# Kernel tuning notes

Measured on AMD Instinct MI355X. Metric: run time of the kernel, lower is better.

## Reference

```python
import jax, jax.numpy as jnp
import numpy as np

NU, NI, D, LAYERS, NNZ = 50000, 50000, 256, 2, 400000
N = NU + NI
LEAKY_ALPHA = 0.2  # tf.nn.leaky_relu default


def setup_inputs() -> dict:
    key = jax.random.key(0)
    ks = jax.random.split(key, 32)
    inp = {}
    inp["initial_ebs"] = jax.random.normal(ks[0], (N, D), jnp.float32) * 0.1
    for i, nm in enumerate(["W_side_u", "W_dot_u", "W_side_i", "W_dot_i"]):
        inp[nm] = jax.random.normal(ks[1 + i], (LAYERS, D, D), jnp.float32) / np.float32(np.sqrt(D))
    vi = 5
    for ent, ne in (("u", NU), ("i", NI)):
        for mat in ("LI", "L"):
            inp[f"{mat}_vals_{ent}"] = jax.random.uniform(ks[vi], (NNZ,), jnp.float32); vi += 1
            inp[f"{mat}_rows_{ent}"] = jnp.sort(jax.random.randint(ks[vi], (NNZ,), 0, ne, jnp.int32)); vi += 1
            inp[f"{mat}_cols_{ent}"] = jax.random.randint(ks[vi], (NNZ,), 0, N, jnp.int32); vi += 1
    return inp


def _spmm(rows, cols, vals, ebs, n_rows):
    # sparse [n_rows, N] @ dense [N, D] via gather + segment-sum
    return jax.ops.segment_sum(vals[:, None] * ebs[cols], rows, num_segments=n_rows)


def reference(initial_ebs, W_side_u, W_dot_u, W_side_i, W_dot_i,
              LI_vals_u, L_vals_u, LI_vals_i, L_vals_i,
              LI_rows_u, LI_cols_u, L_rows_u, L_cols_u,
              LI_rows_i, LI_cols_i, L_rows_i, L_cols_i):
    ebs = initial_ebs
    layers_ebs = []
    for l in range(LAYERS):
        # entity 'u': rows [0, NU)
        li_u = _spmm(LI_rows_u, LI_cols_u, LI_vals_u, ebs, NU)
        l_u = _spmm(L_rows_u, L_cols_u, L_vals_u, ebs, NU)
        fold_u = jax.nn.leaky_relu(li_u @ W_side_u[l] + (l_u * ebs[:NU]) @ W_dot_u[l], LEAKY_ALPHA)
        # entity 'i': rows [NU, N)
        li_i = _spmm(LI_rows_i, LI_cols_i, LI_vals_i, ebs, NI)
        l_i = _spmm(L_rows_i, L_cols_i, L_vals_i, ebs, NI)
        fold_i = jax.nn.leaky_relu(li_i @ W_side_i[l] + (l_i * ebs[NU:]) @ W_dot_i[l], LEAKY_ALPHA)
        ebs = jnp.concatenate([fold_u, fold_i], axis=0)  # [N, D]
        layers_ebs.append(ebs)
    return jnp.concatenate(layers_ebs, axis=0)  # [LAYERS*N, D]
```

## Files before the change

kernel.cpp:

```cpp
#include <hip/hip_runtime.h>

#define NUQ 50000
#define NIQ 50000
#define DQ 256
#define NTOT 100000
#define LALPHA 0.2f
#define GPE 782

typedef __attribute__((ext_vector_type(8))) __bf16 bf16x8;
typedef __attribute__((ext_vector_type(4))) float floatx4;
typedef __attribute__((ext_vector_type(8))) unsigned short ushort8;

__device__ __forceinline__ float b2f(unsigned short u) {
    unsigned int x = ((unsigned int)u) << 16;
    return __builtin_bit_cast(float, x);
}
__device__ __forceinline__ unsigned short f2b(float f) {
    unsigned int u = __builtin_bit_cast(unsigned int, f);
    u = u + 0x7FFFu + ((u >> 16) & 1u);
    return (unsigned short)(u >> 16);
}

#define GLD_LDS16(g, l)                                                        \
    __builtin_amdgcn_global_load_lds(                                          \
        (const __attribute__((address_space(1))) void*)(g),                    \
        (__attribute__((address_space(3))) void*)(l), 16, 0, 0)

__global__ __launch_bounds__(256) void build_rowptr(
    const int* __restrict__ rows, int nnz, int* __restrict__ rptr, int n_rows)
{
    int e = blockIdx.x * 256 + threadIdx.x;
    if (e > nnz) return;
    int prev = (e == 0)   ? -1     : rows[e - 1];
    int cur  = (e == nnz) ? n_rows : rows[e];
    for (int r = prev + 1; r <= cur; ++r) rptr[r] = e;
}

__global__ __launch_bounds__(256) void cvt_f32_bf16(
    const float* __restrict__ in, unsigned short* __restrict__ out, int n4)
{
    int i = blockIdx.x * 256 + threadIdx.x;
    if (i >= n4) return;
    float4 v = ((const float4*)in)[i];
    ushort4 o;
    o.x = f2b(v.x); o.y = f2b(v.y); o.z = f2b(v.z); o.w = f2b(v.w);
    ((ushort4*)out)[i] = o;
}

__global__ __launch_bounds__(256) void build_bt(
    const float* __restrict__ Ws_u, const float* __restrict__ Wd_u,
    const float* __restrict__ Ws_i, const float* __restrict__ Wd_i,
    unsigned short* __restrict__ Bt)
{
    int idx = blockIdx.x * 256 + threadIdx.x;
    int k   = idx & 511;
    int n   = (idx >> 9) & 255;
    int buf = idx >> 17;
    int l = buf >> 1, e = buf & 1;
    const float* Wside = e ? Ws_i : Ws_u;
    const float* Wdot  = e ? Wd_i : Wd_u;
    float v = (k < 256) ? Wside[((size_t)l * 256 + k)       * 256 + n]
                        : Wdot [((size_t)l * 256 + (k-256)) * 256 + n];
    Bt[idx] = f2b(v);
}

__global__ __launch_bounds__(256) void spmm_merged_v3(
    const int* __restrict__ rpA_u, const int* __restrict__ cA_u, const float* __restrict__ vA_u,
    const int* __restrict__ rpB_u, const int* __restrict__ cB_u, const float* __restrict__ vB_u,
    const int* __restrict__ rpA_i, const int* __restrict__ cA_i, const float* __restrict__ vA_i,
    const int* __restrict__ rpB_i, const int* __restrict__ cB_i, const float* __restrict__ vB_i,
    const unsigned short* __restrict__ src,
    unsigned short* __restrict__ out)
{
    const int wave = threadIdx.x >> 6;
    const int lane = threadIdx.x & 63;
    const int r    = __builtin_amdgcn_readfirstlane(blockIdx.x * 4 + wave);
    const bool isI = (r >= NUQ);
    const int  row = isI ? (r - NUQ) : r;

    const int*   rpA = isI ? rpA_i : rpA_u;
    const int*   cAp = isI ? cA_i  : cA_u;
    const float* vAp = isI ? vA_i  : vA_u;
    const int*   rpB = isI ? rpB_i : rpB_u;
    const int*   cBp = isI ? cB_i  : cB_u;
    const float* vBp = isI ? vB_i  : vB_u;

    const int sA = rpA[row], eA = rpA[row + 1];
    const int sB = rpB[row], eB = rpB[row + 1];

    const int half = lane >> 5;
    const int li   = lane & 31;

    float accA[8] = {0.f, 0.f, 0.f, 0.f, 0.f, 0.f, 0.f, 0.f};
    float accB[8] = {0.f, 0.f, 0.f, 0.f, 0.f, 0.f, 0.f, 0.f};

    int baseA = sA, baseB = sB;
    while (baseA < eA || baseB < eB) {
        int cntA = eA - baseA; cntA = cntA < 0 ? 0 : (cntA > 64 ? 64 : cntA);
        int cntB = eB - baseB; cntB = cntB < 0 ? 0 : (cntB > 64 ? 64 : cntB);
        int mycA = 0; float myvA = 0.f;
        if (lane < cntA) { mycA = cAp[baseA + lane]; myvA = vAp[baseA + lane]; }
        int mycB = 0; float myvB = 0.f;
        if (lane < cntB) { mycB = cBp[baseB + lane]; myvB = vBp[baseB + lane]; }
        const int mx = cntA > cntB ? cntA : cntB;
        #pragma unroll 2
        for (int e = 0; e < mx; e += 2) {
            if (e < cntA) {
                const int   c = __shfl(mycA, e + half, 64);
                const float v = __shfl(myvA, e + half, 64);
                const ushort8 s = *(const ushort8*)(src + (size_t)c * DQ + li * 8);
                #pragma unroll
                for (int j = 0; j < 8; ++j) accA[j] = fmaf(v, b2f(s[j]), accA[j]);
            }
            if (e < cntB) {
                const int   c = __shfl(mycB, e + half, 64);
                const float v = __shfl(myvB, e + half, 64);
                const ushort8 s = *(const ushort8*)(src + (size_t)c * DQ + li * 8);
                #pragma unroll
                for (int j = 0; j < 8; ++j) accB[j] = fmaf(v, b2f(s[j]), accB[j]);
            }
        }
        baseA += 64; baseB += 64;
    }

    #pragma unroll
    for (int j = 0; j < 8; ++j) accA[j] += __shfl_xor(accA[j], 32, 64);
    #pragma unroll
    for (int j = 0; j < 8; ++j) accB[j] += __shfl_xor(accB[j], 32, 64);

    float vo[8];
    if (half == 0) {
        #pragma unroll
        for (int j = 0; j < 8; ++j) vo[j] = accA[j];
    } else {
        const ushort8 m = *(const ushort8*)(src + (size_t)r * DQ + li * 8);
        #pragma unroll
        for (int j = 0; j < 8; ++j) vo[j] = accB[j] * b2f(m[j]);
    }
    ushort8 o;
    #pragma unroll
    for (int j = 0; j < 8; ++j) o[j] = f2b(vo[j]);
    *(ushort8*)(out + (size_t)r * 512 + half * 256 + li * 8) = o;
}

__global__ __launch_bounds__(256) void gemm_mfma_leaky_v4(
    const unsigned short* __restrict__ A,
    const unsigned short* __restrict__ Btl,
    float* __restrict__ out,
    unsigned short* __restrict__ ebs,
    const int wb)
{
    __shared__ unsigned short As[32768];
    __shared__ unsigned short Bs[2][8192];

    const int tid  = threadIdx.x;
    const int lane = tid & 63;
    const int w    = tid >> 6;
    const int ent  = (blockIdx.x >= GPE) ? 1 : 0;
    const int bx   = blockIdx.x - ent * GPE;
    const int row0 = ent * NUQ + bx * 64;
    const int Mend = ent * NUQ + NUQ;
    const unsigned short* Bt = Btl + (size_t)ent * 131072;

    const int mA  = ((tid >> 6) << 4) | (tid & 15);
    const int kbA = (tid >> 4) & 3;
    int grs = row0 + mA; if (grs >= Mend) grs = Mend - 1;
    const unsigned short* gA = A + (size_t)grs * 512 + kbA * 8;
    const int ldsA = w * 512;

    const unsigned short* gB[4];
    #pragma unroll
    for (int j = 0; j < 4; ++j) {
        int t = j * 256 + tid;
        int n = ((t >> 6) << 4) | (t & 15);
        gB[j] = Bt + (size_t)n * 512 + ((t >> 4) & 3) * 8;
    }
    const int ldsB = w * 512;

    const int lr  = lane >> 4;
    const int lc  = lane & 15;
    const int gmb = (w & 1) * 2;
    const int gnb = (w >> 1) * 8;

    floatx4 acc[2][8] = {};

    #pragma unroll
    for (int c = 0; c < 16; ++c)
        GLD_LDS16(gA + c * 32, &As[c * 2048 + ldsA]);
    #pragma unroll
    for (int j = 0; j < 4; ++j) GLD_LDS16(gB[j], &Bs[0][j * 2048 + ldsB]);
    #pragma unroll
    for (int j = 0; j < 4; ++j) GLD_LDS16(gB[j] + 32, &Bs[1][j * 2048 + ldsB]);

    for (int kt = 0; kt < 16; ++kt) {
        const int cur = kt & 1;
        if (kt < 15) asm volatile("s_waitcnt vmcnt(4)" ::: "memory");
        else         asm volatile("s_waitcnt vmcnt(0)" ::: "memory");
        __builtin_amdgcn_s_barrier();

        bf16x8 af[2], bfr[8];
        #pragma unroll
        for (int tm = 0; tm < 2; ++tm)
            af[tm] = *(const bf16x8*)&As[kt * 2048 + (gmb + tm) * 512 + lr * 128 + lc * 8];
        #pragma unroll
        for (int tn = 0; tn < 8; ++tn)
            bfr[tn] = *(const bf16x8*)&Bs[cur][(gnb + tn) * 512 + lr * 128 + lc * 8];

        asm volatile("s_waitcnt lgkmcnt(0)" ::: "memory");
        __builtin_amdgcn_s_barrier();

        if (kt < 14) {
            const int ko = (kt + 2) * 32;
            #pragma unroll
            for (int j = 0; j < 4; ++j)
                GLD_LDS16(gB[j] + ko, &Bs[cur][j * 2048 + ldsB]);
        }

        __builtin_amdgcn_s_setprio(1);
        #pragma unroll
        for (int tm = 0; tm < 2; ++tm)
            #pragma unroll
            for (int tn = 0; tn < 8; ++tn)
                acc[tm][tn] = __builtin_amdgcn_mfma_f32_16x16x32_bf16(
                    af[tm], bfr[tn], acc[tm][tn], 0, 0, 0);
        __builtin_amdgcn_s_setprio(0);
    }

    const int m_off = (w & 1) * 32;
    const int n_off = (w >> 1) * 128;
    #pragma unroll
    for (int tm = 0; tm < 2; ++tm) {
        #pragma unroll
        for (int rr = 0; rr < 4; ++rr) {
            const int gr = row0 + m_off + tm * 16 + lr * 4 + rr;
            if (gr >= Mend) continue;
            float*          orow = out + (size_t)gr * 256;
            unsigned short* brow = ebs + (size_t)gr * 256;
            #pragma unroll
            for (int tn = 0; tn < 8; ++tn) {
                const int gc = n_off + tn * 16 + lc;
                float v = acc[tm][tn][rr];
                v = v > 0.f ? v : LALPHA * v;
                orow[gc] = v;
                if (wb) brow[gc] = f2b(v);
            }
        }
    }
}

extern "C" void kernel_launch(void* const* d_in, const int* in_sizes, int n_in,
                              void* d_out, int out_size, void* d_ws, size_t ws_size,
                              hipStream_t stream) {
    const float* ebs0      = (const float*)d_in[0];
    const float* W_side_u  = (const float*)d_in[1];
    const float* W_dot_u   = (const float*)d_in[2];
    const float* W_side_i  = (const float*)d_in[3];
    const float* W_dot_i   = (const float*)d_in[4];
    const float* LI_vals_u = (const float*)d_in[5];
    const int*   LI_rows_u = (const int*)  d_in[6];
    const int*   LI_cols_u = (const int*)  d_in[7];
    const float* L_vals_u  = (const float*)d_in[8];
    const int*   L_rows_u  = (const int*)  d_in[9];
    const int*   L_cols_u  = (const int*)  d_in[10];
    const float* LI_vals_i = (const float*)d_in[11];
    const int*   LI_rows_i = (const int*)  d_in[12];
    const int*   LI_cols_i = (const int*)  d_in[13];
    const float* L_vals_i  = (const float*)d_in[14];
    const int*   L_rows_i  = (const int*)  d_in[15];
    const int*   L_cols_i  = (const int*)  d_in[16];

    float* out = (float*)d_out;

    unsigned short* Abuf   = (unsigned short*)d_ws;
    unsigned short* ebs_bf = (unsigned short*)((char*)d_ws + 102400000);
    unsigned short* Bt     = (unsigned short*)((char*)d_ws + 153600000);
    int* rp_LI_u = (int*)((char*)d_ws + 154648576);
    int* rp_L_u  = rp_LI_u + 50001;
    int* rp_LI_i = rp_L_u  + 50001;
    int* rp_L_i  = rp_LI_i + 50001;

    const int nnz_LI_u = in_sizes[5];
    const int nnz_L_u  = in_sizes[8];
    const int nnz_LI_i = in_sizes[11];
    const int nnz_L_i  = in_sizes[14];

    dim3 b256(256);
    build_rowptr<<<dim3((nnz_LI_u + 256) / 256), b256, 0, stream>>>(LI_rows_u, nnz_LI_u, rp_LI_u, NUQ);
    build_rowptr<<<dim3((nnz_L_u  + 256) / 256), b256, 0, stream>>>(L_rows_u,  nnz_L_u,  rp_L_u,  NUQ);
    build_rowptr<<<dim3((nnz_LI_i + 256) / 256), b256, 0, stream>>>(LI_rows_i, nnz_LI_i, rp_LI_i, NIQ);
    build_rowptr<<<dim3((nnz_L_i  + 256) / 256), b256, 0, stream>>>(L_rows_i,  nnz_L_i,  rp_L_i,  NIQ);
    build_bt<<<dim3(2048), b256, 0, stream>>>(W_side_u, W_dot_u, W_side_i, W_dot_i, Bt);
    cvt_f32_bf16<<<dim3(25000), b256, 0, stream>>>(ebs0, ebs_bf, NTOT * DQ / 4);

    dim3 sgrid(NTOT / 4);
    dim3 ggrid(2 * GPE);

    for (int l = 0; l < 2; ++l) {
        float* outl = out + (size_t)l * NTOT * DQ;
        spmm_merged_v3<<<sgrid, b256, 0, stream>>>(
            rp_LI_u, LI_cols_u, LI_vals_u, rp_L_u, L_cols_u, L_vals_u,
            rp_LI_i, LI_cols_i, LI_vals_i, rp_L_i, L_cols_i, L_vals_i,
            ebs_bf, Abuf);
        gemm_mfma_leaky_v4<<<ggrid, b256, 0, stream>>>(
            Abuf, Bt + (size_t)l * 2 * 131072, outl, ebs_bf, (l == 0) ? 1 : 0);
    }
}
```

Before: 759.6 us.

## Restructure GEMM to stage full B half in LDS, A fragments in registers

The GEMM now uses 512-thread blocks, each computing a 128-row by 128-column tile. The whole K=512 slice of the transposed weights for that column half is loaded into LDS once, and each wave keeps its A fragments in registers, which removes the per-k-step double-buffer barriers. The weight matrix is pre-permuted into an MFMA-friendly layout so LDS fills are contiguous. Block IDs are remapped across 8 groups, likely to spread work across XCDs for better L2 locality. The costs are high register pressure from 16 A fragments per lane, 128KB of LDS per block, and no overlap between loads and compute inside a block.

Result: faster. 684.4 us (-9.9%).

```diff
diff --git a/kernel.cpp b/kernel.cpp
--- a/kernel.cpp
+++ b/kernel.cpp
@@ -5,7 +5,6 @@
 #define DQ 256
 #define NTOT 100000
 #define LALPHA 0.2f
-#define GPE 782
 
 typedef __attribute__((ext_vector_type(8))) __bf16 bf16x8;
 typedef __attribute__((ext_vector_type(4))) float floatx4;
@@ -47,15 +46,23 @@
     ((ushort4*)out)[i] = o;
 }
 
-__global__ __launch_bounds__(256) void build_bt(
+__global__ __launch_bounds__(256) void build_bt_v5(
     const float* __restrict__ Ws_u, const float* __restrict__ Wd_u,
     const float* __restrict__ Ws_i, const float* __restrict__ Wd_i,
     unsigned short* __restrict__ Bt)
 {
     int idx = blockIdx.x * 256 + threadIdx.x;
-    int k   = idx & 511;
-    int n   = (idx >> 9) & 255;
     int buf = idx >> 17;
+    int s2  = idx & 131071;
+    int h   = s2 >> 16;
+    int S   = s2 & 65535;
+    int kt  = S >> 12;
+    int g   = (S >> 9) & 7;
+    int kb  = (S >> 7) & 3;
+    int lc  = (S >> 3) & 15;
+    int j   = S & 7;
+    int n   = h * 128 + g * 16 + lc;
+    int k   = kt * 32 + kb * 8 + j;
     int l = buf >> 1, e = buf & 1;
     const float* Wside = e ? Ws_i : Ws_u;
     const float* Wdot  = e ? Wd_i : Wd_u;
@@ -143,107 +150,77 @@
     *(ushort8*)(out + (size_t)r * 512 + half * 256 + li * 8) = o;
 }
 
-__global__ __launch_bounds__(256) void gemm_mfma_leaky_v4(
+__global__ __launch_bounds__(512, 2) void gemm_mfma_leaky_v5(
     const unsigned short* __restrict__ A,
     const unsigned short* __restrict__ Btl,
     float* __restrict__ out,
     unsigned short* __restrict__ ebs,
     const int wb)
 {
-    __shared__ unsigned short As[32768];
-    __shared__ unsigned short Bs[2][8192];
+    __shared__ unsigned short B_lds[65536];
 
     const int tid  = threadIdx.x;
     const int lane = tid & 63;
     const int w    = tid >> 6;
-    const int ent  = (blockIdx.x >= GPE) ? 1 : 0;
-    const int bx   = blockIdx.x - ent * GPE;
-    const int row0 = ent * NUQ + bx * 64;
+
+    const int orig = blockIdx.x;
+    const int x    = orig & 7;
+    const int kk   = orig >> 3;
+    const int wgid = (x < 4 ? x * 196 : 784 + (x - 4) * 195) + kk;
+
+    const int ent  = (wgid >= 782) ? 1 : 0;
+    const int loc  = wgid - ent * 782;
+    const int rb   = loc >> 1;
+    const int nh   = loc & 1;
+    const int row0 = ent * NUQ + rb * 128;
     const int Mend = ent * NUQ + NUQ;
-    const unsigned short* Bt = Btl + (size_t)ent * 131072;
-
-    const int mA  = ((tid >> 6) << 4) | (tid & 15);
-    const int kbA = (tid >> 4) & 3;
-    int grs = row0 + mA; if (grs >= Mend) grs = Mend - 1;
-    const unsigned short* gA = A + (size_t)grs * 512 + kbA * 8;
-    const int ldsA = w * 512;
-
-    const unsigned short* gB[4];
-    #pragma unroll
-    for (int j = 0; j < 4; ++j) {
-        int t = j * 256 + tid;
-        int n = ((t >> 6) << 4) | (t & 15);
-        gB[j] = Bt + (size_t)n * 512 + ((t >> 4) & 3) * 8;
-    }
-    const int ldsB = w * 512;
-
-    const int lr  = lane >> 4;
-    const int lc  = lane & 15;
-    const int gmb = (w & 1) * 2;
-    const int gnb = (w >> 1) * 8;
-
-    floatx4 acc[2][8] = {};
-
-    #pragma unroll
-    for (int c = 0; c < 16; ++c)
-        GLD_LDS16(gA + c * 32, &As[c * 2048 + ldsA]);
-    #pragma unroll
-    for (int j = 0; j < 4; ++j) GLD_LDS16(gB[j], &Bs[0][j * 2048 + ldsB]);
-    #pragma unroll
-    for (int j = 0; j < 4; ++j) GLD_LDS16(gB[j] + 32, &Bs[1][j * 2048 + ldsB]);
-
+    const unsigned short* BtH = Btl + (size_t)ent * 131072 + (size_t)nh * 65536;
+
+    const int lr = lane >> 4;
+    const int lc = lane & 15;
+
+    #pragma unroll
+    for (int i = 0; i < 16; ++i) {
+        const int t0 = i * 512 + w * 64;
+        GLD_LDS16(BtH + (size_t)(t0 + lane) * 8, &B_lds[t0 * 8]);
+    }
+
+    int grow = row0 + w * 16 + lc;
+    if (grow >= Mend) grow = Mend - 1;
+    const unsigned short* aRow = A + (size_t)grow * 512 + lr * 8;
+    bf16x8 af[16];
+    #pragma unroll
+    for (int kt = 0; kt < 16; ++kt)
+        af[kt] = *(const bf16x8*)(aRow + kt * 32);
+
+    asm volatile("s_waitcnt vmcnt(0)" ::: "memory");
+    __syncthreads();
+
+    floatx4 acc[8] = {};
+    #pragma unroll
     for (int kt = 0; kt < 16; ++kt) {
-        const int cur = kt & 1;
-        if (kt < 15) asm volatile("s_waitcnt vmcnt(4)" ::: "memory");
-        else         asm volatile("s_waitcnt vmcnt(0)" ::: "memory");
-        __builtin_amdgcn_s_barrier();
-
-        bf16x8 af[2], bfr[8];
-        #pragma unroll
-        for (int tm = 0; tm < 2; ++tm)
-            af[tm] = *(const bf16x8*)&As[kt * 2048 + (gmb + tm) * 512 + lr * 128 + lc * 8];
-        #pragma unroll
-        for (int tn = 0; tn < 8; ++tn)
-            bfr[tn] = *(const bf16x8*)&Bs[cur][(gnb + tn) * 512 + lr * 128 + lc * 8];
-
-        asm volatile("s_waitcnt lgkmcnt(0)" ::: "memory");
-        __builtin_amdgcn_s_barrier();
-
-        if (kt < 14) {
-            const int ko = (kt + 2) * 32;
-            #pragma unroll
-            for (int j = 0; j < 4; ++j)
-                GLD_LDS16(gB[j] + ko, &Bs[cur][j * 2048 + ldsB]);
+        #pragma unroll
+        for (int tn = 0; tn < 8; ++tn) {
+            const bf16x8 bfr = *(const bf16x8*)
+                &B_lds[kt * 4096 + tn * 512 + lr * 128 + lc * 8];
+            acc[tn] = __builtin_amdgcn_mfma_f32_16x16x32_bf16(
+                af[kt], bfr, acc[tn], 0, 0, 0);
         }
-
-        __builtin_amdgcn_s_setprio(1);
-        #pragma unroll
-        for (int tm = 0; tm < 2; ++tm)
-            #pragma unroll
-            for (int tn = 0; tn < 8; ++tn)
-                acc[tm][tn] = __builtin_amdgcn_mfma_f32_16x16x32_bf16(
-                    af[tm], bfr[tn], acc[tm][tn], 0, 0, 0);
-        __builtin_amdgcn_s_setprio(0);
-    }
-
-    const int m_off = (w & 1) * 32;
-    const int n_off = (w >> 1) * 128;
-    #pragma unroll
-    for (int tm = 0; tm < 2; ++tm) {
-        #pragma unroll
-        for (int rr = 0; rr < 4; ++rr) {
-            const int gr = row0 + m_off + tm * 16 + lr * 4 + rr;
-            if (gr >= Mend) continue;
-            float*          orow = out + (size_t)gr * 256;
-            unsigned short* brow = ebs + (size_t)gr * 256;
-            #pragma unroll
-            for (int tn = 0; tn < 8; ++tn) {
-                const int gc = n_off + tn * 16 + lc;
-                float v = acc[tm][tn][rr];
-                v = v > 0.f ? v : LALPHA * v;
-                orow[gc] = v;
-                if (wb) brow[gc] = f2b(v);
-            }
+    }
+
+    #pragma unroll
+    for (int rr = 0; rr < 4; ++rr) {
+        const int gr = row0 + w * 16 + lr * 4 + rr;
+        if (gr >= Mend) continue;
+        float*          orow = out + (size_t)gr * 256;
+        unsigned short* brow = ebs + (size_t)gr * 256;
+        #pragma unroll
+        for (int tn = 0; tn < 8; ++tn) {
+            const int gc = nh * 128 + tn * 16 + lc;
+            float v = acc[tn][rr];
+            v = v > 0.f ? v : LALPHA * v;
+            orow[gc] = v;
+            if (wb) brow[gc] = f2b(v);
         }
     }
 }
@@ -289,11 +266,12 @@
     build_rowptr<<<dim3((nnz_L_u  + 256) / 256), b256, 0, stream>>>(L_rows_u,  nnz_L_u,  rp_L_u,  NUQ);
     build_rowptr<<<dim3((nnz_LI_i + 256) / 256), b256, 0, stream>>>(LI_rows_i, nnz_LI_i, rp_LI_i, NIQ);
     build_rowptr<<<dim3((nnz_L_i  + 256) / 256), b256, 0, stream>>>(L_rows_i,  nnz_L_i,  rp_L_i,  NIQ);
-    build_bt<<<dim3(2048), b256, 0, stream>>>(W_side_u, W_dot_u, W_side_i, W_dot_i, Bt);
+    build_bt_v5<<<dim3(2048), b256, 0, stream>>>(W_side_u, W_dot_u, W_side_i, W_dot_i, Bt);
     cvt_f32_bf16<<<dim3(25000), b256, 0, stream>>>(ebs0, ebs_bf, NTOT * DQ / 4);
 
     dim3 sgrid(NTOT / 4);
-    dim3 ggrid(2 * GPE);
+    dim3 ggrid(1564);
+    dim3 b512(512);
 
     for (int l = 0; l < 2; ++l) {
         float* outl = out + (size_t)l * NTOT * DQ;
@@ -301,7 +279,7 @@
             rp_LI_u, LI_cols_u, LI_vals_u, rp_L_u, L_cols_u, L_vals_u,
             rp_LI_i, LI_cols_i, LI_vals_i, rp_L_i, L_cols_i, L_vals_i,
             ebs_bf, Abuf);
-        gemm_mfma_leaky_v4<<<ggrid, b256, 0, stream>>>(
+        gemm_mfma_leaky_v5<<<ggrid, b512, 0, stream>>>(
             Abuf, Bt + (size_t)l * 2 * 131072, outl, ebs_bf, (l == 0) ? 1 : 0);
     }
 }
```
